# Optimization experiments

Measured on AMD Instinct MI355X. Metric: run time of the kernel, lower is better.

## Reference

```python
import jax, jax.numpy as jnp
import numpy as np

D_MODEL = 1024
N_SEQ = 2048
H = 16


def _rope_tables(d, n_seq):
    # theta_i = 10000^(-2i/d), i in [0, d/2)
    i = jnp.arange(d // 2, dtype=jnp.float32)
    theta = jnp.power(10000.0, -2.0 * i / d)                 # [d/2]
    ang = jnp.arange(n_seq, dtype=jnp.float32)[:, None] * theta[None, :]  # [S, d/2]
    cos = jnp.repeat(jnp.cos(ang), 2, axis=-1)               # [S, d] (cos duplicated per pair)
    s = jnp.sin(ang)
    sin = jnp.stack([s, -s], axis=-1).reshape(n_seq, d)      # [S, d] (+sin, -sin interleaved)
    return cos, sin


def _apply_rope(x, cos, sin):
    d = x.shape[-1]
    # swap adjacent pairs: (x0,x1,x2,x3,...) -> (x1,x0,x3,x2,...)
    x2 = x.reshape(x.shape[:-1] + (d // 2, 2))[..., ::-1].reshape(x.shape)
    return x * cos + x2 * sin


def setup_inputs() -> dict:
    key = jax.random.key(0)
    ks = jax.random.split(key, 8)
    B, S, D = 2, N_SEQ, D_MODEL
    scale = 1.0 / np.sqrt(D)
    return {
        "q": jax.random.normal(ks[0], (B, S, D), dtype=jnp.float32),
        "k": jax.random.normal(ks[1], (B, S, D), dtype=jnp.float32),
        "v": jax.random.normal(ks[2], (B, S, D), dtype=jnp.float32),
        "W_q": jax.random.normal(ks[3], (D, D), dtype=jnp.float32) * scale,
        "W_k": jax.random.normal(ks[4], (D, D), dtype=jnp.float32) * scale,
        "W_v": jax.random.normal(ks[5], (D, D), dtype=jnp.float32) * scale,
        "W_o": jax.random.normal(ks[6], (D, D), dtype=jnp.float32) * scale,
        "b_o": jax.random.normal(ks[7], (D,), dtype=jnp.float32) * scale,
    }


def reference(q, k, v, W_q, W_k, W_v, W_o, b_o):
    B, S, D = q.shape
    d_k = D // H
    cos, sin = _rope_tables(D, N_SEQ)

    query = _apply_rope(q @ W_q.T, cos, sin)  # RoPE over full d_model, pre head-split
    key_ = _apply_rope(k @ W_k.T, cos, sin)
    value = v @ W_v.T

    def split_heads(x):
        return x.reshape(B, S, H, d_k).transpose(0, 2, 1, 3)  # [B,H,S,dk]

    qh, kh, vh = split_heads(query), split_heads(key_), split_heads(value)

    scores = jnp.einsum("bhsd,bhtd->bhst", qh, kh) / jnp.sqrt(jnp.float32(d_k))
    attn = jax.nn.softmax(scores, axis=-1)
    y = jnp.einsum("bhst,bhtd->bhsd", attn, vh)               # [B,H,S,dk]
    y = y.transpose(0, 2, 1, 3).reshape(B, S, D)
    return y @ W_o.T + b_o
```

## Files before the change

kernel.cpp:

```cpp
#include <hip/hip_runtime.h>
#include <hip/hip_bf16.h>

using bf16 = __hip_bfloat16;
using bf16x8 = __attribute__((ext_vector_type(8))) short;
using f32x4 = __attribute__((ext_vector_type(4))) float;

#define LOG2E 1.44269504088896f

__device__ __forceinline__ void gload_lds16(const void* g, void* lds) {
    __builtin_amdgcn_global_load_lds(
        (const __attribute__((address_space(1))) void*)g,
        (__attribute__((address_space(3))) void*)lds, 16, 0, 0);
}

struct __align__(16) BH8 { bf16 h[8]; };
struct __align__(8)  BH4 { bf16 h[4]; };

struct CvtArgs { const float* src[7]; BH8* dst[7]; };

__global__ __launch_bounds__(256) void cvt_rope(CvtArgs ca,
        float* __restrict__ ct, float* __restrict__ st) {
    int bid = blockIdx.x;
    if (bid < 8192) {
        int i = bid * 256 + threadIdx.x;
        const float* src; BH8* dst; int off;
        if (i < 3 * 524288) {
            int w = i >> 19; off = i & 524287;
            src = ca.src[w]; dst = ca.dst[w];
        } else {
            int j = i - 3 * 524288;
            int w = 3 + (j >> 17); off = j & 131071;
            src = ca.src[w]; dst = ca.dst[w];
        }
        const float4* p = (const float4*)src + (size_t)off * 2;
        float4 a = p[0], b = p[1];
        BH8 r;
        r.h[0] = __float2bfloat16(a.x); r.h[1] = __float2bfloat16(a.y);
        r.h[2] = __float2bfloat16(a.z); r.h[3] = __float2bfloat16(a.w);
        r.h[4] = __float2bfloat16(b.x); r.h[5] = __float2bfloat16(b.y);
        r.h[6] = __float2bfloat16(b.z); r.h[7] = __float2bfloat16(b.w);
        dst[off] = r;
    } else {
        int idx = (bid - 8192) * 256 + threadIdx.x;
        if (idx >= 2048 * 512) return;
        int s = idx >> 9, i = idx & 511;
        float theta = exp2f((float)i * -0.0259525632413075f);
        float ang = (float)s * theta;
        ct[idx] = cosf(ang);
        st[idx] = sinf(ang);
    }
}

struct ProjArgs {
    const bf16* A[3];
    const bf16* W[3];
    void* out[3];
    int mode[3];
};

template <int MF>
__global__ __launch_bounds__(256, (MF == 4 ? 3 : 2)) void gemm_bt(ProjArgs pa,
        const float* __restrict__ ct, const float* __restrict__ st,
        const float* __restrict__ bias) {
    constexpr int Kd = 1024;
    constexpr int BM = MF * 32;
    __shared__ __align__(16) bf16 As[BM * 64];
    __shared__ __align__(16) bf16 Bs[128 * 64];
    const int z = blockIdx.z;
    const bf16* __restrict__ A = pa.A[z];
    const bf16* __restrict__ W = pa.W[z];
    const int mode = pa.mode[z];
    const int tid = threadIdx.x, wid = tid >> 6, lane = tid & 63;
    const int g = lane >> 4, l15 = lane & 15;
    const int wm = wid >> 1, wn = wid & 1;
    const int m0 = blockIdx.y * BM, n0 = blockIdx.x * 128;
    f32x4 acc[MF][4] = {};

    const int sbyte = tid * 16;

    for (int kb = 0; kb < Kd; kb += 64) {
        __syncthreads();
#pragma unroll
        for (int i = 0; i < MF; ++i) {
            int byte = sbyte + i * 4096;
            int row = byte >> 7, cb = byte & 127;
            int csrc = cb ^ ((row & 7) << 4);
            gload_lds16((const char*)(A + (size_t)(m0 + row) * Kd + kb) + csrc,
                        (char*)As + wid * 1024 + i * 4096);
        }
#pragma unroll
        for (int i = 0; i < 4; ++i) {
            int byte = sbyte + i * 4096;
            int row = byte >> 7, cb = byte & 127;
            int csrc = cb ^ ((row & 7) << 4);
            gload_lds16((const char*)(W + (size_t)(n0 + row) * Kd + kb) + csrc,
                        (char*)Bs + wid * 1024 + i * 4096);
        }
        __syncthreads();
        bf16x8 af[MF][2], bw[4][2];
#pragma unroll
        for (int i = 0; i < MF; ++i) {
            int ra = wm * (MF * 16) + i * 16 + l15;
#pragma unroll
            for (int kk = 0; kk < 2; ++kk)
                af[i][kk] = *(const bf16x8*)((const char*)As + ra * 128 +
                                             ((kk * 64 + g * 16) ^ ((ra & 7) << 4)));
        }
#pragma unroll
        for (int j = 0; j < 4; ++j) {
            int rb = wn * 64 + j * 16 + l15;
#pragma unroll
            for (int kk = 0; kk < 2; ++kk)
                bw[j][kk] = *(const bf16x8*)((const char*)Bs + rb * 128 +
                                             ((kk * 64 + g * 16) ^ ((rb & 7) << 4)));
        }
#pragma unroll
        for (int kk = 0; kk < 2; ++kk)
#pragma unroll
            for (int i = 0; i < MF; ++i)
#pragma unroll
                for (int j = 0; j < 4; ++j)
                    acc[i][j] = __builtin_amdgcn_mfma_f32_16x16x32_bf16(
                        af[i][kk], bw[j][kk], acc[i][j], 0, 0, 0);
    }

    if (mode == 0) {
        float* out = (float*)pa.out[z];
#pragma unroll
        for (int i = 0; i < MF; ++i) {
            int row = m0 + wm * (MF * 16) + i * 16 + g * 4;
#pragma unroll
            for (int j = 0; j < 4; ++j) {
                int col = n0 + wn * 64 + j * 16 + l15;
                float bv = bias[col];
#pragma unroll
                for (int r = 0; r < 4; ++r)
                    out[(size_t)(row + r) * 1024 + col] = acc[i][j][r] + bv;
            }
        }
    } else if (mode == 3) {
        bf16* out = (bf16*)pa.out[z];
#pragma unroll
        for (int i = 0; i < MF; ++i) {
            int m = m0 + wm * (MF * 16) + i * 16 + g * 4;
            int b = m >> 11, s = m & 2047;
#pragma unroll
            for (int j = 0; j < 4; ++j) {
                int col = n0 + wn * 64 + j * 16 + l15;
                int h = col >> 6, dv = col & 63;
                BH4 pk;
#pragma unroll
                for (int r = 0; r < 4; ++r) pk.h[r] = __float2bfloat16(acc[i][j][r]);
                *(BH4*)(out + (((size_t)(b * 16 + h)) * 64 + dv) * 2048 + s) = pk;
            }
        }
    } else {
        bf16* out = (bf16*)pa.out[z];
        float scl = (mode == 1) ? (0.125f * LOG2E) : 1.0f;
#pragma unroll
        for (int i = 0; i < MF; ++i) {
            int mrow = m0 + wm * (MF * 16) + i * 16 + g * 4;
#pragma unroll
            for (int j = 0; j < 4; ++j) {
                int col = n0 + wn * 64 + j * 16 + l15;
                int ci = col >> 1;
                float sgn = (col & 1) ? -1.0f : 1.0f;
                int h = col >> 6, dv = col & 63;
#pragma unroll
                for (int r = 0; r < 4; ++r) {
                    int m = mrow + r;
                    int b = m >> 11, s = m & 2047;
                    float vv = acc[i][j][r];
                    float pv = __shfl_xor(vv, 1);
                    float c = ct[s * 512 + ci], sn = st[s * 512 + ci];
                    float o = (vv * c + sgn * sn * pv) * scl;
                    out[(((size_t)(b * 16 + h)) * 2048 + s) * 64 + dv] = __float2bfloat16(o);
                }
            }
        }
    }
}

__global__ __launch_bounds__(128, 2) void attn_fwd(
        const bf16* __restrict__ Qh, const bf16* __restrict__ Kh,
        const bf16* __restrict__ Vt, bf16* __restrict__ Y) {
    __shared__ __align__(16) bf16 Ks[2][64 * 64];
    const int tid = threadIdx.x, wid = tid >> 6, lane = tid & 63;
    const int g = lane >> 4, l15 = lane & 15;
    const int lin = blockIdx.y * 32 + blockIdx.x;
    const int swz = (lin & 7) * 128 + (lin >> 3);
    const int bh = swz >> 5, qt = swz & 31;
    const int q0 = qt * 64 + wid * 32;
    const bf16* Qb = Qh + (size_t)bh * 2048 * 64;
    const bf16* Kb = Kh + (size_t)bh * 2048 * 64;
    const bf16* Vb = Vt + (size_t)bh * 64 * 2048;

    bf16x8 aq[2][2];
#pragma unroll
    for (int qfr = 0; qfr < 2; ++qfr)
#pragma unroll
        for (int kk = 0; kk < 2; ++kk)
            aq[qfr][kk] = *(const bf16x8*)(Qb + (size_t)(q0 + qfr * 16 + l15) * 64 + kk * 32 + g * 8);

    f32x4 yacc[2][4] = {};
    float lrow[2] = {0.f, 0.f};

    int csrc[4], kphys[4];
#pragma unroll
    for (int i = 0; i < 4; ++i) {
        int byte = tid * 16 + i * 2048;
        int L = byte >> 7;
        csrc[i] = (byte & 127) ^ ((L & 7) << 4);
        kphys[i] = ((L >> 5) << 5) + (((L >> 2) & 3) << 3) + (((L >> 4) & 1) << 2) + (L & 3);
    }

#define STAGE(T, BUF)                                                          \
    do {                                                                       \
        _Pragma("unroll")                                                      \
        for (int i = 0; i < 4; ++i)                                            \
            gload_lds16((const char*)(Kb + (size_t)((T) * 64 + kphys[i]) * 64) + csrc[i], \
                        (char*)&Ks[BUF][0] + tid * 16 + i * 2048);             \
    } while (0)

    STAGE(0, 0);

    for (int t = 0; t < 32; ++t) {
        __syncthreads();

        bf16x8 vf[4][2];
#pragma unroll
        for (int dn = 0; dn < 4; ++dn)
#pragma unroll
            for (int ch = 0; ch < 2; ++ch)
                vf[dn][ch] = *(const bf16x8*)(Vb + (size_t)(dn * 16 + l15) * 2048 +
                                              t * 64 + ch * 32 + g * 8);
        if (t < 31) STAGE(t + 1, (t + 1) & 1);
        __builtin_amdgcn_sched_barrier(0);

        const char* Kst = (const char*)&Ks[t & 1][0];

        f32x4 sacc[4][2] = {};
#pragma unroll
        for (int kk = 0; kk < 2; ++kk) {
            bf16x8 kf[4];
#pragma unroll
            for (int kfr = 0; kfr < 4; ++kfr)
                kf[kfr] = *(const bf16x8*)(Kst + (kfr * 16 + l15) * 128 +
                                           ((kk * 64 + g * 16) ^ ((l15 & 7) << 4)));
#pragma unroll
            for (int kfr = 0; kfr < 4; ++kfr)
#pragma unroll
                for (int qfr = 0; qfr < 2; ++qfr)
                    sacc[kfr][qfr] = __builtin_amdgcn_mfma_f32_16x16x32_bf16(
                        kf[kfr], aq[qfr][kk], sacc[kfr][qfr], 0, 0, 0);
        }

        bf16x8 ap[2][2];
#pragma unroll
        for (int qfr = 0; qfr < 2; ++qfr)
#pragma unroll
            for (int ch = 0; ch < 2; ++ch) {
                bf16 hh[8];
#pragma unroll
                for (int r = 0; r < 4; ++r) {
                    float x = exp2f(sacc[2 * ch][qfr][r]);
                    lrow[qfr] += x;
                    hh[r] = __float2bfloat16(x);
                }
#pragma unroll
                for (int r = 0; r < 4; ++r) {
                    float x = exp2f(sacc[2 * ch + 1][qfr][r]);
                    lrow[qfr] += x;
                    hh[4 + r] = __float2bfloat16(x);
                }
                ap[qfr][ch] = *(const bf16x8*)hh;
            }

#pragma unroll
        for (int ch = 0; ch < 2; ++ch)
#pragma unroll
            for (int qfr = 0; qfr < 2; ++qfr)
#pragma unroll
                for (int dn = 0; dn < 4; ++dn)
                    yacc[qfr][dn] = __builtin_amdgcn_mfma_f32_16x16x32_bf16(
                        ap[qfr][ch], vf[dn][ch], yacc[qfr][dn], 0, 0, 0);
    }
#undef STAGE

    const int b = bh >> 4, h = bh & 15;
#pragma unroll
    for (int qfr = 0; qfr < 2; ++qfr) {
        float ls = lrow[qfr];
        ls += __shfl_xor(ls, 16);
        ls += __shfl_xor(ls, 32);
#pragma unroll
        for (int r = 0; r < 4; ++r) {
            float lv = __shfl(ls, g * 4 + r);
            float inv = 1.0f / lv;
            int s = q0 + qfr * 16 + g * 4 + r;
            bf16* yp = Y + ((size_t)(b * 2048 + s)) * 1024 + h * 64;
#pragma unroll
            for (int dn = 0; dn < 4; ++dn)
                yp[dn * 16 + l15] = __float2bfloat16(yacc[qfr][dn][r] * inv);
        }
    }
}

extern "C" void kernel_launch(void* const* d_in, const int* in_sizes, int n_in,
                              void* d_out, int out_size, void* d_ws, size_t ws_size,
                              hipStream_t stream) {
    const float* q  = (const float*)d_in[0];
    const float* k  = (const float*)d_in[1];
    const float* v  = (const float*)d_in[2];
    const float* Wq = (const float*)d_in[3];
    const float* Wk = (const float*)d_in[4];
    const float* Wv = (const float*)d_in[5];
    const float* Wo = (const float*)d_in[6];
    const float* bo = (const float*)d_in[7];

    const size_t MB = 1048576ull;
    if (ws_size < 72 * MB) return;
    char* p = (char*)d_ws;
    bf16* qb  = (bf16*)(p + 0 * MB);
    bf16* kb  = (bf16*)(p + 8 * MB);
    bf16* vb  = (bf16*)(p + 16 * MB);
    bf16* Wqb = (bf16*)(p + 24 * MB);
    bf16* Wkb = (bf16*)(p + 26 * MB);
    bf16* Wvb = (bf16*)(p + 28 * MB);
    bf16* Wob = (bf16*)(p + 30 * MB);
    bf16* Qh  = (bf16*)(p + 32 * MB);
    bf16* Kh  = (bf16*)(p + 40 * MB);
    bf16* Vt  = (bf16*)(p + 48 * MB);
    bf16* Yb  = (bf16*)(p + 56 * MB);
    float* ct = (float*)(p + 64 * MB);
    float* st = (float*)(p + 68 * MB);

    CvtArgs ca;
    ca.src[0] = q;  ca.dst[0] = (BH8*)qb;
    ca.src[1] = k;  ca.dst[1] = (BH8*)kb;
    ca.src[2] = v;  ca.dst[2] = (BH8*)vb;
    ca.src[3] = Wq; ca.dst[3] = (BH8*)Wqb;
    ca.src[4] = Wk; ca.dst[4] = (BH8*)Wkb;
    ca.src[5] = Wv; ca.dst[5] = (BH8*)Wvb;
    ca.src[6] = Wo; ca.dst[6] = (BH8*)Wob;
    cvt_rope<<<12288, 256, 0, stream>>>(ca, ct, st);

    ProjArgs pa;
    pa.A[0] = qb;  pa.A[1] = kb;  pa.A[2] = vb;
    pa.W[0] = Wqb; pa.W[1] = Wkb; pa.W[2] = Wvb;
    pa.out[0] = Qh; pa.out[1] = Kh; pa.out[2] = Vt;
    pa.mode[0] = 1; pa.mode[1] = 2; pa.mode[2] = 3;
    gemm_bt<4><<<dim3(8, 32, 3), 256, 0, stream>>>(pa, ct, st, nullptr);

    attn_fwd<<<dim3(32, 32), 128, 0, stream>>>(Qh, Kh, Vt, Yb);

    ProjArgs pf;
    pf.A[0] = Yb; pf.A[1] = Yb; pf.A[2] = Yb;
    pf.W[0] = Wob; pf.W[1] = Wob; pf.W[2] = Wob;
    pf.out[0] = d_out; pf.out[1] = d_out; pf.out[2] = d_out;
    pf.mode[0] = 0; pf.mode[1] = 0; pf.mode[2] = 0;
    gemm_bt<2><<<dim3(8, 64, 1), 256, 0, stream>>>(pf, ct, st, bo);
}
```

Measured before the change: 162.8 us.

## Process two K/V tiles per iteration with four-deep LDS K buffering

Restructures the attention main loop to handle two 64-key tiles per iteration, using four LDS K buffers and prefetching two tiles ahead. This halves the number of barriers and lets the QK^T MFMAs of the second tile overlap the softmax of the first, meant to cut synchronisation and latency stalls. In exchange it doubles LDS usage to 32KB per block and raises register pressure (two sets of V fragments and score accumulators), which could spill or reduce occupancy under launch_bounds(128,2).

```diff
diff --git a/kernel.cpp b/kernel.cpp
--- a/kernel.cpp
+++ b/kernel.cpp
@@ -184,7 +184,7 @@
 __global__ __launch_bounds__(128, 2) void attn_fwd(
         const bf16* __restrict__ Qh, const bf16* __restrict__ Kh,
         const bf16* __restrict__ Vt, bf16* __restrict__ Y) {
-    __shared__ __align__(16) bf16 Ks[2][64 * 64];
+    __shared__ __align__(16) bf16 Ks[4][64 * 64];
     const int tid = threadIdx.x, wid = tid >> 6, lane = tid & 63;
     const int g = lane >> 4, l15 = lane & 15;
     const int lin = blockIdx.y * 32 + blockIdx.x;
@@ -214,78 +214,99 @@
         kphys[i] = ((L >> 5) << 5) + (((L >> 2) & 3) << 3) + (((L >> 4) & 1) << 2) + (L & 3);
     }
 
-#define STAGE(T, BUF)                                                          \
+#define STAGE(T)                                                               \
     do {                                                                       \
         _Pragma("unroll")                                                      \
         for (int i = 0; i < 4; ++i)                                            \
             gload_lds16((const char*)(Kb + (size_t)((T) * 64 + kphys[i]) * 64) + csrc[i], \
-                        (char*)&Ks[BUF][0] + tid * 16 + i * 2048);             \
+                        (char*)&Ks[(T) & 3][0] + tid * 16 + i * 2048);         \
     } while (0)
 
-    STAGE(0, 0);
-
-    for (int t = 0; t < 32; ++t) {
+#define QKT(KST, SACC)                                                         \
+    do {                                                                       \
+        _Pragma("unroll")                                                      \
+        for (int kk = 0; kk < 2; ++kk) {                                       \
+            bf16x8 kf[4];                                                      \
+            _Pragma("unroll")                                                  \
+            for (int kfr = 0; kfr < 4; ++kfr)                                  \
+                kf[kfr] = *(const bf16x8*)((KST) + (kfr * 16 + l15) * 128 +    \
+                                           ((kk * 64 + g * 16) ^ ((l15 & 7) << 4))); \
+            _Pragma("unroll")                                                  \
+            for (int kfr = 0; kfr < 4; ++kfr)                                  \
+                _Pragma("unroll")                                              \
+                for (int qfr = 0; qfr < 2; ++qfr)                              \
+                    SACC[kfr][qfr] = __builtin_amdgcn_mfma_f32_16x16x32_bf16(  \
+                        kf[kfr], aq[qfr][kk], SACC[kfr][qfr], 0, 0, 0);        \
+        }                                                                      \
+    } while (0)
+
+#define SOFTMAX_PV(SACC, VF)                                                   \
+    do {                                                                       \
+        bf16x8 ap[2][2];                                                       \
+        _Pragma("unroll")                                                      \
+        for (int qfr = 0; qfr < 2; ++qfr)                                      \
+            _Pragma("unroll")                                                  \
+            for (int ch = 0; ch < 2; ++ch) {                                   \
+                bf16 hh[8];                                                    \
+                _Pragma("unroll")                                              \
+                for (int r = 0; r < 4; ++r) {                                  \
+                    float x = exp2f(SACC[2 * ch][qfr][r]);                     \
+                    lrow[qfr] += x;                                            \
+                    hh[r] = __float2bfloat16(x);                               \
+                }                                                              \
+                _Pragma("unroll")                                              \
+                for (int r = 0; r < 4; ++r) {                                  \
+                    float x = exp2f(SACC[2 * ch + 1][qfr][r]);                 \
+                    lrow[qfr] += x;                                            \
+                    hh[4 + r] = __float2bfloat16(x);                           \
+                }                                                              \
+                ap[qfr][ch] = *(const bf16x8*)hh;                              \
+            }                                                                  \
+        _Pragma("unroll")                                                      \
+        for (int ch = 0; ch < 2; ++ch)                                         \
+            _Pragma("unroll")                                                  \
+            for (int qfr = 0; qfr < 2; ++qfr)                                  \
+                _Pragma("unroll")                                              \
+                for (int dn = 0; dn < 4; ++dn)                                 \
+                    yacc[qfr][dn] = __builtin_amdgcn_mfma_f32_16x16x32_bf16(   \
+                        ap[qfr][ch], VF[dn][ch], yacc[qfr][dn], 0, 0, 0);      \
+    } while (0)
+
+    STAGE(0);
+    STAGE(1);
+
+    for (int i = 0; i < 16; ++i) {
+        const int t0 = 2 * i, t1 = 2 * i + 1;
         __syncthreads();
 
-        bf16x8 vf[4][2];
+        bf16x8 vf0[4][2], vf1[4][2];
 #pragma unroll
         for (int dn = 0; dn < 4; ++dn)
 #pragma unroll
             for (int ch = 0; ch < 2; ++ch)
-                vf[dn][ch] = *(const bf16x8*)(Vb + (size_t)(dn * 16 + l15) * 2048 +
-                                              t * 64 + ch * 32 + g * 8);
-        if (t < 31) STAGE(t + 1, (t + 1) & 1);
+                vf0[dn][ch] = *(const bf16x8*)(Vb + (size_t)(dn * 16 + l15) * 2048 +
+                                               t0 * 64 + ch * 32 + g * 8);
+#pragma unroll
+        for (int dn = 0; dn < 4; ++dn)
+#pragma unroll
+            for (int ch = 0; ch < 2; ++ch)
+                vf1[dn][ch] = *(const bf16x8*)(Vb + (size_t)(dn * 16 + l15) * 2048 +
+                                               t1 * 64 + ch * 32 + g * 8);
+        if (i < 15) { STAGE(t0 + 2); STAGE(t1 + 2); }
         __builtin_amdgcn_sched_barrier(0);
 
-        const char* Kst = (const char*)&Ks[t & 1][0];
-
-        f32x4 sacc[4][2] = {};
-#pragma unroll
-        for (int kk = 0; kk < 2; ++kk) {
-            bf16x8 kf[4];
-#pragma unroll
-            for (int kfr = 0; kfr < 4; ++kfr)
-                kf[kfr] = *(const bf16x8*)(Kst + (kfr * 16 + l15) * 128 +
-                                           ((kk * 64 + g * 16) ^ ((l15 & 7) << 4)));
-#pragma unroll
-            for (int kfr = 0; kfr < 4; ++kfr)
-#pragma unroll
-                for (int qfr = 0; qfr < 2; ++qfr)
-                    sacc[kfr][qfr] = __builtin_amdgcn_mfma_f32_16x16x32_bf16(
-                        kf[kfr], aq[qfr][kk], sacc[kfr][qfr], 0, 0, 0);
-        }
-
-        bf16x8 ap[2][2];
-#pragma unroll
-        for (int qfr = 0; qfr < 2; ++qfr)
-#pragma unroll
-            for (int ch = 0; ch < 2; ++ch) {
-                bf16 hh[8];
-#pragma unroll
-                for (int r = 0; r < 4; ++r) {
-                    float x = exp2f(sacc[2 * ch][qfr][r]);
-                    lrow[qfr] += x;
-                    hh[r] = __float2bfloat16(x);
-                }
-#pragma unroll
-                for (int r = 0; r < 4; ++r) {
-                    float x = exp2f(sacc[2 * ch + 1][qfr][r]);
-                    lrow[qfr] += x;
-                    hh[4 + r] = __float2bfloat16(x);
-                }
-                ap[qfr][ch] = *(const bf16x8*)hh;
-            }
-
-#pragma unroll
-        for (int ch = 0; ch < 2; ++ch)
-#pragma unroll
-            for (int qfr = 0; qfr < 2; ++qfr)
-#pragma unroll
-                for (int dn = 0; dn < 4; ++dn)
-                    yacc[qfr][dn] = __builtin_amdgcn_mfma_f32_16x16x32_bf16(
-                        ap[qfr][ch], vf[dn][ch], yacc[qfr][dn], 0, 0, 0);
+        const char* Kst0 = (const char*)&Ks[t0 & 3][0];
+        const char* Kst1 = (const char*)&Ks[t1 & 3][0];
+
+        f32x4 sacc0[4][2] = {}, sacc1[4][2] = {};
+        QKT(Kst0, sacc0);
+        QKT(Kst1, sacc1);
+        SOFTMAX_PV(sacc0, vf0);
+        SOFTMAX_PV(sacc1, vf1);
     }
 #undef STAGE
+#undef QKT
+#undef SOFTMAX_PV
 
     const int b = bh >> 4, h = bh & 15;
 #pragma unroll
```

New measurement: 189.7 us. +16.5%, slower.
